# Kernel optimization log

Hardware: AMD Instinct MI355X
Metric: run time of the kernel (lower is better)

The kernel has to match this reference:

```python
import jax, jax.numpy as jnp
import numpy as np

ASPECT = 1.0
SCALE = 0.3
MIN_PATCH_H = 60.0
EPS = 1e-6


def _make_patch_boxes(boxes, H, W):
    # Patcher.create: per detected box, compute [ymin_patch, xmin_patch, patch_h, patch_w]
    ymin, xmin, ymax, xmax = jnp.split(boxes, 4, axis=-1)
    h = ymax - ymin
    w = xmax - xmin
    pw = h * SCALE
    ph = ASPECT * pw
    oy = ymin + h / 2.0
    ox = xmin + w / 2.0
    yp = jnp.maximum(oy - ph / 2.0, 0.0)
    xp = jnp.maximum(ox - pw / 2.0, 0.0)
    yp = jnp.where(yp + ph > H, H - ph, yp)
    xp = jnp.where(xp + pw > W, W - pw, xp)
    return jnp.concatenate([yp, xp, ph, pw], axis=-1)  # [B, N, 4]


def _bilinear(src, rel_y, rel_x, out_h, out_w):
    # tf.image.resize bilinear (half-pixel centers): sample src [P,P,3] at the
    # grid of an (out_h, out_w) resize, evaluated at all H/W image offsets.
    P = src.shape[0]
    sy = jnp.clip((rel_y + 0.5) * P / out_h - 0.5, 0.0, P - 1.0)  # [H]
    sx = jnp.clip((rel_x + 0.5) * P / out_w - 0.5, 0.0, P - 1.0)  # [W]
    y0 = jnp.floor(sy).astype(jnp.int32); y1 = jnp.minimum(y0 + 1, P - 1)
    x0 = jnp.floor(sx).astype(jnp.int32); x1 = jnp.minimum(x0 + 1, P - 1)
    wy = (sy - y0.astype(sy.dtype))[:, None, None]
    wx = (sx - x0.astype(sx.dtype))[None, :, None]
    top = (1.0 - wx) * src[y0[:, None], x0[None, :]] + wx * src[y0[:, None], x1[None, :]]
    bot = (1.0 - wx) * src[y1[:, None], x0[None, :]] + wx * src[y1[:, None], x1[None, :]]
    return (1.0 - wy) * top + wy * bot  # [H, W, 3]


def _forward(images, boxes, patch):
    B, H, W, _ = images.shape
    pboxes = _make_patch_boxes(boxes, float(H), float(W))  # [B, N, 4]
    valid = pboxes[..., 2] > MIN_PATCH_H                    # gather_nd filter
    p_mean = patch.mean((0, 1))
    p_std = patch.std((0, 1)) + EPS
    ys = jnp.arange(H, dtype=jnp.int32)
    xs = jnp.arange(W, dtype=jnp.int32)

    def per_image(image, pbs, vls):
        # serial while_loop over patches: later patches overwrite earlier ones,
        # and histogram match uses the current (already-patched) background.
        def step(img, bv):
            pb, v = bv
            pbi = pb.astype(jnp.int32)  # tf.cast truncation
            y0, x0, ph, pw = pbi[0], pbi[1], pbi[2], pbi[3]
            in_y = (ys >= y0) & (ys < y0 + ph)
            in_x = (xs >= x0) & (xs < x0 + pw)
            mask = in_y[:, None] & in_x[None, :]            # [H, W]
            mf = mask[..., None].astype(img.dtype)
            cnt = jnp.maximum(mask.sum().astype(img.dtype), 1.0)
            bg_mean = (img * mf).sum((0, 1)) / cnt
            bg_std = jnp.sqrt((((img - bg_mean) ** 2) * mf).sum((0, 1)) / cnt) + EPS
            # histogram match (per-channel moment matching) of patch to background
            matched = (patch - p_mean) / p_std * bg_std + bg_mean
            phf = jnp.maximum(ph.astype(img.dtype), 1.0)
            pwf = jnp.maximum(pw.astype(img.dtype), 1.0)
            sampled = _bilinear(matched,
                                (ys - y0).astype(img.dtype),
                                (xs - x0).astype(img.dtype), phf, pwf)
            img = jnp.where(mask[..., None] & v, sampled, img)
            return img, None

        img, _ = jax.lax.scan(step, image, (pbs, vls))
        return img

    return jax.vmap(per_image)(images, pboxes, valid)


def setup_inputs() -> dict:
    key = jax.random.key(0)
    k1, k2, k3 = jax.random.split(key, 3)
    B, N, H, W, P = 16, 16, 512, 512, 512
    images = jax.random.normal(k1, (B, H, W, 3), dtype=jnp.float32)
    u = jax.random.uniform(k2, (B, N, 4), dtype=jnp.float32)
    ymin = u[..., 0] * (H - 320)
    xmin = u[..., 1] * (W - 320)
    h = 150.0 + u[..., 2] * 150.0
    w = 150.0 + u[..., 3] * 150.0
    boxes = jnp.stack([ymin, xmin, ymin + h, xmin + w], axis=-1)
    patch = jax.random.normal(k3, (P, P, 3), dtype=jnp.float32) * 0.5
    return {"images": images, "boxes": boxes, "patch": patch}


def reference(images, boxes, patch):
    return _forward(images, boxes, patch)
```

## Files before the change

kernel.cpp:

```cpp
#include <hip/hip_runtime.h>
#include <math.h>

#define IMG_H 512
#define IMG_W 512
#define PSIZE 512
#define NIMG 16
#define NBOX 16
#define Z0 8
#define SLOTS 24
#define NTASK (256 * 17 * Z0)
#define NCOPY 2048
#define CHUNK4 1536
#define FBLOCKS 4096

#define WS_PMEAN 0
#define WS_PSTD  3
#define WS_PART  6
#define WS_PAIR  1544
#define WS_COEF  (1544 + 256 * SLOTS * 8)

typedef float f4u __attribute__((ext_vector_type(4), aligned(4)));
typedef float f2u __attribute__((ext_vector_type(2), aligned(4)));

struct BoxGeo { int y0, x0, ph, pw, valid; };

__device__ __forceinline__ BoxGeo make_geo(const float* bx) {
    float ymin = bx[0], xmin = bx[1], ymax = bx[2], xmax = bx[3];
    float h = ymax - ymin, w = xmax - xmin;
    float pwf = h * 0.3f;
    float phf = 1.0f * pwf;
    float oy = ymin + h * 0.5f;
    float ox = xmin + w * 0.5f;
    float yp = fmaxf(oy - phf * 0.5f, 0.0f);
    float xp = fmaxf(ox - pwf * 0.5f, 0.0f);
    if (yp + phf > (float)IMG_H) yp = (float)IMG_H - phf;
    if (xp + pwf > (float)IMG_W) xp = (float)IMG_W - pwf;
    BoxGeo g;
    g.y0 = (int)yp; g.x0 = (int)xp;
    g.ph = (int)phf; g.pw = (int)pwf;
    g.valid = (phf > 60.0f) ? 1 : 0;
    return g;
}

__device__ __forceinline__ void bsample_fast(const float* __restrict__ patch,
                                             int relY, int relX,
                                             float phf, float pwf, float s[3]) {
    float sy = ((float)relY + 0.5f) * (float)PSIZE / phf - 0.5f;
    sy = fminf(fmaxf(sy, 0.0f), (float)(PSIZE - 1));
    float sx = ((float)relX + 0.5f) * (float)PSIZE / pwf - 0.5f;
    sx = fminf(fmaxf(sx, 0.0f), (float)(PSIZE - 1));
    int y0 = (int)floorf(sy);
    int y1 = min(y0 + 1, PSIZE - 1);
    int x0 = (int)floorf(sx);
    float wy = sy - (float)y0;
    float wx = sx - (float)x0;
    const int baseX = min(x0, PSIZE - 2);
    const bool hi = (x0 == PSIZE - 1);
    const float* r0 = patch + (y0 * PSIZE + baseX) * 3;
    const float* r1 = patch + (y1 * PSIZE + baseX) * 3;
    f4u a0 = *(const f4u*)r0; f2u b0 = *(const f2u*)(r0 + 4);
    f4u a1 = *(const f4u*)r1; f2u b1 = *(const f2u*)(r1 + 4);
    float p00, p01, p10, p11, top, bot;
    p00 = hi ? a0.w : a0.x;  p01 = a0.w;
    p10 = hi ? a1.w : a1.x;  p11 = a1.w;
    top = (1.f - wx) * p00 + wx * p01; bot = (1.f - wx) * p10 + wx * p11;
    s[0] = (1.f - wy) * top + wy * bot;
    p00 = hi ? b0.x : a0.y;  p01 = b0.x;
    p10 = hi ? b1.x : a1.y;  p11 = b1.x;
    top = (1.f - wx) * p00 + wx * p01; bot = (1.f - wx) * p10 + wx * p11;
    s[1] = (1.f - wy) * top + wy * bot;
    p00 = hi ? b0.y : a0.z;  p01 = b0.y;
    p10 = hi ? b1.y : a1.z;  p11 = b1.y;
    top = (1.f - wx) * p00 + wx * p01; bot = (1.f - wx) * p10 + wx * p11;
    s[2] = (1.f - wy) * top + wy * bot;
}

template<int N, int NWAVES>
__device__ __forceinline__ void block_reduceN(float v[N]) {
    __shared__ float lds[NWAVES][N];
    const int lane = threadIdx.x & 63;
    const int wave = threadIdx.x >> 6;
    __syncthreads();
#pragma unroll
    for (int k = 0; k < N; ++k) {
#pragma unroll
        for (int off = 32; off > 0; off >>= 1)
            v[k] += __shfl_down(v[k], off, 64);
    }
    if (lane == 0) {
#pragma unroll
        for (int k = 0; k < N; ++k) lds[wave][k] = v[k];
    }
    __syncthreads();
    if (wave == 0) {
#pragma unroll
        for (int k = 0; k < N; ++k) {
            float x = (lane < NWAVES) ? lds[lane][k] : 0.0f;
#pragma unroll
            for (int off = 32; off > 0; off >>= 1)
                x += __shfl_down(x, off, 64);
            if (lane == 0) lds[0][k] = x;
        }
    }
    __syncthreads();
#pragma unroll
    for (int k = 0; k < N; ++k) v[k] = lds[0][k];
}

__global__ void patch_stats_partial(const float* __restrict__ patch,
                                    float* __restrict__ ws) {
    const int g = blockIdx.x * 256 + threadIdx.x;
    const float4* p4 = (const float4*)patch;
    float4 a = p4[3 * g], b = p4[3 * g + 1], c = p4[3 * g + 2];
    float v[6];
    v[0] = a.x + a.w + b.z + c.y;
    v[1] = a.y + b.x + b.w + c.z;
    v[2] = a.z + b.y + c.x + c.w;
    v[3] = a.x*a.x + a.w*a.w + b.z*b.z + c.y*c.y;
    v[4] = a.y*a.y + b.x*b.x + b.w*b.w + c.z*c.z;
    v[5] = a.z*a.z + b.y*b.y + c.x*c.x + c.w*c.w;
    block_reduceN<6, 4>(v);
    if (threadIdx.x == 0) {
        float* o = ws + WS_PART + blockIdx.x * 6;
#pragma unroll
        for (int k = 0; k < 6; ++k) o[k] = v[k];
    }
}

__launch_bounds__(256)
__global__ void fused(const float* __restrict__ images,
                      const float* __restrict__ boxes,
                      const float* __restrict__ patch,
                      float* __restrict__ ws,
                      float* __restrict__ out) {
    const int tid = threadIdx.x;
    __shared__ BoxGeo geo[NBOX];
    const int total = NTASK + NCOPY + 1;

    for (int it = blockIdx.x; it < total; it += FBLOCKS) {
        if (it >= NTASK) {
            if (it < NTASK + NCOPY) {
                const int c = it - NTASK;
                const float4* s4 = (const float4*)images;
                float4* d4 = (float4*)out;
                const int base = c * CHUNK4 + tid;
#pragma unroll
                for (int u = 0; u < 6; ++u)
                    d4[base + u * 256] = s4[base + u * 256];
            } else {
                float v[6];
                const float* p = ws + WS_PART + tid * 6;
#pragma unroll
                for (int k = 0; k < 6; ++k) v[k] = p[k];
                block_reduceN<6, 4>(v);
                if (tid == 0) {
                    const float n = (float)(PSIZE * PSIZE);
#pragma unroll
                    for (int c = 0; c < 3; ++c) {
                        float m = v[c] / n;
                        float var = v[3 + c] / n - m * m;
                        ws[WS_PMEAN + c] = m;
                        ws[WS_PSTD + c] = sqrtf(fmaxf(var, 0.f)) + 1e-6f;
                    }
                }
            }
            continue;
        }
        const int z = it / (17 * 256);
        const int rem = it % (17 * 256);
        const int j_idx = rem >> 8;
        const int bi = rem & 255;
        const int b = bi >> 4, i = bi & 15;
        if (j_idx > i) continue;
        if (j_idx >= 1 && z > 0) continue;

        const BoxGeo gi = make_geo(boxes + (b * NBOX + i) * 4);
        if (!gi.valid) continue;

        const int slot = (j_idx == 0) ? z : (Z0 + j_idx - 1);
        float* o = ws + WS_PAIR + ((size_t)bi * SLOTS + slot) * 8;

        int ry0 = gi.y0, rx0 = gi.x0;
        int ry1 = gi.y0 + gi.ph, rx1 = gi.x0 + gi.pw;
        int jy0 = 0, jx0 = 0, jph = -1;
        float jphf = 1.f, jpwf = 1.f;
        if (j_idx >= 1) {
            const BoxGeo gj = make_geo(boxes + (b * NBOX + j_idx - 1) * 4);
            if (!gj.valid) {
                if (tid == 0) { for (int k = 0; k < 7; ++k) o[k] = 0.f; }
                continue;
            }
            ry0 = max(ry0, gj.y0); rx0 = max(rx0, gj.x0);
            ry1 = min(ry1, gj.y0 + gj.ph); rx1 = min(rx1, gj.x0 + gj.pw);
            jy0 = gj.y0; jx0 = gj.x0; jph = gj.ph;
            jphf = (float)gj.ph; jpwf = (float)gj.pw;
        }
        const int rw = rx1 - rx0, rh = ry1 - ry0;
        if (rw <= 0 || rh <= 0) {
            if (tid == 0) { for (int k = 0; k < 7; ++k) o[k] = 0.f; }
            continue;
        }

        __syncthreads();
        if (tid < NBOX)
            geo[tid] = make_geo(boxes + (b * NBOX + tid) * 4);
        __syncthreads();

        const int n = rw * rh;
        const float* img = images + (size_t)b * IMG_H * IMG_W * 3;
        const int nz = (j_idx == 0) ? Z0 : 1;

        float v[7] = {0.f, 0.f, 0.f, 0.f, 0.f, 0.f, 0.f};
        for (int t = z * 256 + tid; t < n; t += 256 * nz) {
            const int y = ry0 + t / rw;
            const int x = rx0 + t % rw;
            bool inc = true;
            for (int k = j_idx; k < i; ++k) {
                const BoxGeo gk = geo[k];
                if (gk.valid && y >= gk.y0 && y < gk.y0 + gk.ph &&
                    x >= gk.x0 && x < gk.x0 + gk.pw) { inc = false; break; }
            }
            if (inc) {
                float s[3];
                if (jph > 0) {
                    bsample_fast(patch, y - jy0, x - jx0, jphf, jpwf, s);
                } else {
                    const float* p = img + ((size_t)y * IMG_W + x) * 3;
                    s[0] = p[0]; s[1] = p[1]; s[2] = p[2];
                }
                v[0] += 1.f;
                v[1] += s[0]; v[2] += s[1]; v[3] += s[2];
                v[4] += s[0]*s[0]; v[5] += s[1]*s[1]; v[6] += s[2]*s[2];
            }
        }
        block_reduceN<7, 4>(v);
        if (tid == 0) {
#pragma unroll
            for (int k = 0; k < 7; ++k) o[k] = v[k];
        }
    }
}

__global__ void solve_coeffs(const float* __restrict__ boxes,
                             float* __restrict__ ws) {
    const int b = blockIdx.x;
    const int lane = threadIdx.x;

    BoxGeo g = make_geo(boxes + (b * NBOX + (lane < NBOX ? lane : NBOX - 1)) * 4);
    float pm[3], ps[3];
#pragma unroll
    for (int c = 0; c < 3; ++c) { pm[c] = ws[WS_PMEAN + c]; ps[c] = ws[WS_PSTD + c]; }

    float sc[3] = {0.f, 0.f, 0.f}, of[3] = {0.f, 0.f, 0.f};

    for (int i = 0; i < NBOX; ++i) {
        const int valid_i = __shfl(g.valid, i, 64);
        if (!valid_i) continue;

        float cnt = 0.f, s1[3] = {0.f,0.f,0.f}, s2[3] = {0.f,0.f,0.f};
        if (lane <= i) {
            const int slot0 = (lane == 0) ? 0 : (Z0 + lane - 1);
            const int nz = (lane == 0) ? Z0 : 1;
            const float* p = ws + WS_PAIR +
                ((size_t)(b * NBOX + i) * SLOTS + slot0) * 8;
            for (int zz = 0; zz < nz; ++zz) {
                cnt   += p[zz*8 + 0];
                s1[0] += p[zz*8 + 1]; s1[1] += p[zz*8 + 2]; s1[2] += p[zz*8 + 3];
                s2[0] += p[zz*8 + 4]; s2[1] += p[zz*8 + 5]; s2[2] += p[zz*8 + 6];
            }
        }
        float ts[3], tq[3];
#pragma unroll
        for (int c = 0; c < 3; ++c) {
            if (lane == 0) { ts[c] = s1[c]; tq[c] = s2[c]; }
            else {
                ts[c] = sc[c] * s1[c] + of[c] * cnt;
                tq[c] = sc[c]*sc[c]*s2[c] + 2.f*sc[c]*of[c]*s1[c] + of[c]*of[c]*cnt;
            }
        }
#pragma unroll
        for (int c = 0; c < 3; ++c) {
#pragma unroll
            for (int off = 16; off > 0; off >>= 1) {
                ts[c] += __shfl_down(ts[c], off, 32);
                tq[c] += __shfl_down(tq[c], off, 32);
            }
        }
        const int phi = __shfl(g.ph, i, 64);
        const int pwi = __shfl(g.pw, i, 64);
        const float cntf = fmaxf((float)(phi * pwi), 1.0f);
        float nsc[3] = {0.f,0.f,0.f}, nof[3] = {0.f,0.f,0.f};
        if (lane == 0) {
#pragma unroll
            for (int c = 0; c < 3; ++c) {
                float mean = ts[c] / cntf;
                float var = tq[c] / cntf - mean * mean;
                float sd = sqrtf(fmaxf(var, 0.f)) + 1e-6f;
                nsc[c] = sd / ps[c];
                nof[c] = mean - pm[c] * nsc[c];
            }
        }
#pragma unroll
        for (int c = 0; c < 3; ++c) {
            float bs = __shfl(nsc[c], 0, 64);
            float bo = __shfl(nof[c], 0, 64);
            if (lane == i + 1) { sc[c] = bs; of[c] = bo; }
            if (lane == 0) {
                ws[WS_COEF + (size_t)(b * NBOX + i) * 8 + c] = bs;
                ws[WS_COEF + (size_t)(b * NBOX + i) * 8 + 3 + c] = bo;
            }
        }
    }
}

__launch_bounds__(256)
__global__ void decal(const float* __restrict__ boxes,
                      const float* __restrict__ patch,
                      const float* __restrict__ ws,
                      float* __restrict__ out) {
    const int bi = blockIdx.x;
    const int b = bi >> 4, i = bi & 15;
    const int z = blockIdx.y;
    __shared__ BoxGeo geo[NBOX];
    __shared__ float coef[6];
    if (threadIdx.x < NBOX)
        geo[threadIdx.x] = make_geo(boxes + (b * NBOX + threadIdx.x) * 4);
    if (threadIdx.x >= 32 && threadIdx.x < 38)
        coef[threadIdx.x - 32] = ws[WS_COEF + (size_t)bi * 8 + (threadIdx.x - 32)];
    __syncthreads();
    const BoxGeo gi = geo[i];
    if (!gi.valid) return;
    const int y0 = gi.y0, x0 = gi.x0, ph = gi.ph, pw = gi.pw;
    const int n = ph * pw;
    const float phf = (float)ph, pwf = (float)pw;
    float* img = out + (size_t)b * IMG_H * IMG_W * 3;

    for (int t = z * 256 + threadIdx.x; t < n; t += 256 * 8) {
        const int y = y0 + t / pw;
        const int x = x0 + t % pw;
        bool cov = false;
        for (int k = i + 1; k < NBOX; ++k) {
            const BoxGeo g = geo[k];
            if (g.valid && y >= g.y0 && y < g.y0 + g.ph &&
                x >= g.x0 && x < g.x0 + g.pw) { cov = true; break; }
        }
        if (!cov) {
            float s[3];
            bsample_fast(patch, y - y0, x - x0, phf, pwf, s);
            float* o = img + ((size_t)y * IMG_W + x) * 3;
            o[0] = s[0] * coef[0] + coef[3];
            o[1] = s[1] * coef[1] + coef[4];
            o[2] = s[2] * coef[2] + coef[5];
        }
    }
}

extern "C" void kernel_launch(void* const* d_in, const int* in_sizes, int n_in,
                              void* d_out, int out_size, void* d_ws, size_t ws_size,
                              hipStream_t stream) {
    const float* images = (const float*)d_in[0];
    const float* boxes  = (const float*)d_in[1];
    const float* patch  = (const float*)d_in[2];
    float* out = (float*)d_out;
    float* ws  = (float*)d_ws;

    patch_stats_partial<<<256, 256, 0, stream>>>(patch, ws);
    fused<<<FBLOCKS, 256, 0, stream>>>(images, boxes, patch, ws, out);
    solve_coeffs<<<NIMG, 64, 0, stream>>>(boxes, ws);
    decal<<<dim3(NIMG * NBOX, 8), 256, 0, stream>>>(boxes, patch, ws, out);
}
```

Baseline: 116.9 us.

## Merge four kernels into two and compact the fused task list

Folds the patch-statistics partial reduction into the first fused kernel as extra work items. It also replaces the sparse (z, j, bi) task grid, which had many early-exit items, with a dense enumeration: 8-way split tasks for the background stats plus 120 triangular pair tasks per image. The coefficient solve is merged into the decal kernel, so every decal block redundantly recomputes the final patch stats and the serial per-image coefficient chain up to its own box. This cuts two launches and removes wasted no-op iterations, at the cost of duplicated solve work in each of the 8 z-blocks per box.

```diff
diff --git a/kernel.cpp b/kernel.cpp
--- a/kernel.cpp
+++ b/kernel.cpp
@@ -8,16 +8,15 @@
 #define NBOX 16
 #define Z0 8
 #define SLOTS 24
-#define NTASK (256 * 17 * Z0)
-#define NCOPY 2048
-#define CHUNK4 1536
+#define IT_J0   256
+#define IT_PAIR 2304
+#define IT_COPY 4224
+#define NITEMS  6272
 #define FBLOCKS 4096
-
-#define WS_PMEAN 0
-#define WS_PSTD  3
-#define WS_PART  6
-#define WS_PAIR  1544
-#define WS_COEF  (1544 + 256 * SLOTS * 8)
+#define CHUNK4  1536
+
+#define WS_PART 0
+#define WS_PAIR 1536
 
 typedef float f4u __attribute__((ext_vector_type(4), aligned(4)));
 typedef float f2u __attribute__((ext_vector_type(2), aligned(4)));
@@ -107,85 +106,70 @@
     for (int k = 0; k < N; ++k) v[k] = lds[0][k];
 }
 
-__global__ void patch_stats_partial(const float* __restrict__ patch,
-                                    float* __restrict__ ws) {
-    const int g = blockIdx.x * 256 + threadIdx.x;
-    const float4* p4 = (const float4*)patch;
-    float4 a = p4[3 * g], b = p4[3 * g + 1], c = p4[3 * g + 2];
-    float v[6];
-    v[0] = a.x + a.w + b.z + c.y;
-    v[1] = a.y + b.x + b.w + c.z;
-    v[2] = a.z + b.y + c.x + c.w;
-    v[3] = a.x*a.x + a.w*a.w + b.z*b.z + c.y*c.y;
-    v[4] = a.y*a.y + b.x*b.x + b.w*b.w + c.z*c.z;
-    v[5] = a.z*a.z + b.y*b.y + c.x*c.x + c.w*c.w;
-    block_reduceN<6, 4>(v);
-    if (threadIdx.x == 0) {
-        float* o = ws + WS_PART + blockIdx.x * 6;
-#pragma unroll
-        for (int k = 0; k < 6; ++k) o[k] = v[k];
-    }
-}
-
 __launch_bounds__(256)
-__global__ void fused(const float* __restrict__ images,
-                      const float* __restrict__ boxes,
-                      const float* __restrict__ patch,
-                      float* __restrict__ ws,
-                      float* __restrict__ out) {
+__global__ void fused1(const float* __restrict__ images,
+                       const float* __restrict__ boxes,
+                       const float* __restrict__ patch,
+                       float* __restrict__ ws,
+                       float* __restrict__ out) {
     const int tid = threadIdx.x;
     __shared__ BoxGeo geo[NBOX];
-    const int total = NTASK + NCOPY + 1;
-
-    for (int it = blockIdx.x; it < total; it += FBLOCKS) {
-        if (it >= NTASK) {
-            if (it < NTASK + NCOPY) {
-                const int c = it - NTASK;
-                const float4* s4 = (const float4*)images;
-                float4* d4 = (float4*)out;
-                const int base = c * CHUNK4 + tid;
-#pragma unroll
-                for (int u = 0; u < 6; ++u)
-                    d4[base + u * 256] = s4[base + u * 256];
-            } else {
-                float v[6];
-                const float* p = ws + WS_PART + tid * 6;
-#pragma unroll
-                for (int k = 0; k < 6; ++k) v[k] = p[k];
-                block_reduceN<6, 4>(v);
-                if (tid == 0) {
-                    const float n = (float)(PSIZE * PSIZE);
-#pragma unroll
-                    for (int c = 0; c < 3; ++c) {
-                        float m = v[c] / n;
-                        float var = v[3 + c] / n - m * m;
-                        ws[WS_PMEAN + c] = m;
-                        ws[WS_PSTD + c] = sqrtf(fmaxf(var, 0.f)) + 1e-6f;
-                    }
-                }
+
+    for (int it = blockIdx.x; it < NITEMS; it += FBLOCKS) {
+        if (it < IT_J0) {
+            const int g = it * 256 + tid;
+            const float4* p4 = (const float4*)patch;
+            float4 a = p4[3 * g], b = p4[3 * g + 1], c = p4[3 * g + 2];
+            float v[6];
+            v[0] = a.x + a.w + b.z + c.y;
+            v[1] = a.y + b.x + b.w + c.z;
+            v[2] = a.z + b.y + c.x + c.w;
+            v[3] = a.x*a.x + a.w*a.w + b.z*b.z + c.y*c.y;
+            v[4] = a.y*a.y + b.x*b.x + b.w*b.w + c.z*c.z;
+            v[5] = a.z*a.z + b.y*b.y + c.x*c.x + c.w*c.w;
+            block_reduceN<6, 4>(v);
+            if (tid == 0) {
+                float* o = ws + WS_PART + it * 6;
+#pragma unroll
+                for (int k = 0; k < 6; ++k) o[k] = v[k];
             }
             continue;
         }
-        const int z = it / (17 * 256);
-        const int rem = it % (17 * 256);
-        const int j_idx = rem >> 8;
-        const int bi = rem & 255;
-        const int b = bi >> 4, i = bi & 15;
-        if (j_idx > i) continue;
-        if (j_idx >= 1 && z > 0) continue;
-
+        if (it >= IT_COPY) {
+            const int c = it - IT_COPY;
+            const float4* s4 = (const float4*)images;
+            float4* d4 = (float4*)out;
+            const int base = c * CHUNK4 + tid;
+#pragma unroll
+            for (int u = 0; u < 6; ++u)
+                d4[base + u * 256] = s4[base + u * 256];
+            continue;
+        }
+        int b, i, j, z;
+        if (it < IT_PAIR) {
+            const int idx = it - IT_J0;
+            const int bi = idx >> 3; z = idx & 7;
+            b = bi >> 4; i = bi & 15; j = -1;
+        } else {
+            const int idx = it - IT_PAIR;
+            b = idx / 120;
+            int p = idx % 120;
+            int pi = 1, t = p;
+            while (t >= pi) { t -= pi; ++pi; }
+            i = pi; j = t; z = 0;
+        }
         const BoxGeo gi = make_geo(boxes + (b * NBOX + i) * 4);
         if (!gi.valid) continue;
 
-        const int slot = (j_idx == 0) ? z : (Z0 + j_idx - 1);
-        float* o = ws + WS_PAIR + ((size_t)bi * SLOTS + slot) * 8;
+        const int slot = (j < 0) ? z : (Z0 + j);
+        float* o = ws + WS_PAIR + ((size_t)(b * NBOX + i) * SLOTS + slot) * 8;
 
         int ry0 = gi.y0, rx0 = gi.x0;
         int ry1 = gi.y0 + gi.ph, rx1 = gi.x0 + gi.pw;
         int jy0 = 0, jx0 = 0, jph = -1;
         float jphf = 1.f, jpwf = 1.f;
-        if (j_idx >= 1) {
-            const BoxGeo gj = make_geo(boxes + (b * NBOX + j_idx - 1) * 4);
+        if (j >= 0) {
+            const BoxGeo gj = make_geo(boxes + (b * NBOX + j) * 4);
             if (!gj.valid) {
                 if (tid == 0) { for (int k = 0; k < 7; ++k) o[k] = 0.f; }
                 continue;
@@ -208,14 +192,14 @@
 
         const int n = rw * rh;
         const float* img = images + (size_t)b * IMG_H * IMG_W * 3;
-        const int nz = (j_idx == 0) ? Z0 : 1;
+        const int stride = (j < 0) ? 256 * Z0 : 256;
 
         float v[7] = {0.f, 0.f, 0.f, 0.f, 0.f, 0.f, 0.f};
-        for (int t = z * 256 + tid; t < n; t += 256 * nz) {
+        for (int t = ((j < 0) ? z * 256 : 0) + tid; t < n; t += stride) {
             const int y = ry0 + t / rw;
             const int x = rx0 + t % rw;
             bool inc = true;
-            for (int k = j_idx; k < i; ++k) {
+            for (int k = j + 1; k < i; ++k) {
                 const BoxGeo gk = geo[k];
                 if (gk.valid && y >= gk.y0 && y < gk.y0 + gk.ph &&
                     x >= gk.x0 && x < gk.x0 + gk.pw) { inc = false; break; }
@@ -241,101 +225,113 @@
     }
 }
 
-__global__ void solve_coeffs(const float* __restrict__ boxes,
-                             float* __restrict__ ws) {
-    const int b = blockIdx.x;
-    const int lane = threadIdx.x;
-
-    BoxGeo g = make_geo(boxes + (b * NBOX + (lane < NBOX ? lane : NBOX - 1)) * 4);
-    float pm[3], ps[3];
-#pragma unroll
-    for (int c = 0; c < 3; ++c) { pm[c] = ws[WS_PMEAN + c]; ps[c] = ws[WS_PSTD + c]; }
-
-    float sc[3] = {0.f, 0.f, 0.f}, of[3] = {0.f, 0.f, 0.f};
-
-    for (int i = 0; i < NBOX; ++i) {
-        const int valid_i = __shfl(g.valid, i, 64);
-        if (!valid_i) continue;
-
-        float cnt = 0.f, s1[3] = {0.f,0.f,0.f}, s2[3] = {0.f,0.f,0.f};
-        if (lane <= i) {
-            const int slot0 = (lane == 0) ? 0 : (Z0 + lane - 1);
-            const int nz = (lane == 0) ? Z0 : 1;
-            const float* p = ws + WS_PAIR +
-                ((size_t)(b * NBOX + i) * SLOTS + slot0) * 8;
-            for (int zz = 0; zz < nz; ++zz) {
-                cnt   += p[zz*8 + 0];
-                s1[0] += p[zz*8 + 1]; s1[1] += p[zz*8 + 2]; s1[2] += p[zz*8 + 3];
-                s2[0] += p[zz*8 + 4]; s2[1] += p[zz*8 + 5]; s2[2] += p[zz*8 + 6];
-            }
-        }
-        float ts[3], tq[3];
+__launch_bounds__(256)
+__global__ void solve_decal(const float* __restrict__ boxes,
+                            const float* __restrict__ patch,
+                            const float* __restrict__ ws,
+                            float* __restrict__ out) {
+    const int bi = blockIdx.x;
+    const int z = blockIdx.y;
+    const int b = bi >> 4, i = bi & 15;
+    const int tid = threadIdx.x;
+    __shared__ BoxGeo geo[NBOX];
+    __shared__ float scoef[6];
+
+    if (tid < NBOX)
+        geo[tid] = make_geo(boxes + (b * NBOX + tid) * 4);
+    __syncthreads();
+    if (!geo[i].valid) return;
+
+    if (tid < 64) {
+        const int lane = tid;
+        float v[6] = {0.f, 0.f, 0.f, 0.f, 0.f, 0.f};
+        for (int q = lane; q < 256; q += 64) {
+            const float* p = ws + WS_PART + q * 6;
+#pragma unroll
+            for (int k = 0; k < 6; ++k) v[k] += p[k];
+        }
+#pragma unroll
+        for (int k = 0; k < 6; ++k)
+#pragma unroll
+            for (int off = 32; off > 0; off >>= 1)
+                v[k] += __shfl_xor(v[k], off, 64);
+        const float n = (float)(PSIZE * PSIZE);
+        float pm[3], ps[3];
 #pragma unroll
         for (int c = 0; c < 3; ++c) {
-            if (lane == 0) { ts[c] = s1[c]; tq[c] = s2[c]; }
-            else {
-                ts[c] = sc[c] * s1[c] + of[c] * cnt;
-                tq[c] = sc[c]*sc[c]*s2[c] + 2.f*sc[c]*of[c]*s1[c] + of[c]*of[c]*cnt;
-            }
-        }
-#pragma unroll
-        for (int c = 0; c < 3; ++c) {
-#pragma unroll
-            for (int off = 16; off > 0; off >>= 1) {
-                ts[c] += __shfl_down(ts[c], off, 32);
-                tq[c] += __shfl_down(tq[c], off, 32);
-            }
-        }
-        const int phi = __shfl(g.ph, i, 64);
-        const int pwi = __shfl(g.pw, i, 64);
-        const float cntf = fmaxf((float)(phi * pwi), 1.0f);
-        float nsc[3] = {0.f,0.f,0.f}, nof[3] = {0.f,0.f,0.f};
-        if (lane == 0) {
+            pm[c] = v[c] / n;
+            ps[c] = sqrtf(fmaxf(v[3 + c] / n - pm[c] * pm[c], 0.f)) + 1e-6f;
+        }
+
+        BoxGeo g = geo[lane & 15];
+        float sc[3] = {0.f, 0.f, 0.f}, of[3] = {0.f, 0.f, 0.f};
+
+        for (int ii = 0; ii <= i; ++ii) {
+            const int valid_i = __shfl(g.valid, ii, 64);
+            if (!valid_i) continue;
+
+            float cnt = 0.f, s1[3] = {0.f,0.f,0.f}, s2[3] = {0.f,0.f,0.f};
+            if (lane <= ii) {
+                const int slot0 = (lane == 0) ? 0 : (Z0 + lane - 1);
+                const int nzz = (lane == 0) ? Z0 : 1;
+                const float* p = ws + WS_PAIR +
+                    ((size_t)(b * NBOX + ii) * SLOTS + slot0) * 8;
+                for (int zz = 0; zz < nzz; ++zz) {
+                    cnt   += p[zz*8 + 0];
+                    s1[0] += p[zz*8 + 1]; s1[1] += p[zz*8 + 2]; s1[2] += p[zz*8 + 3];
+                    s2[0] += p[zz*8 + 4]; s2[1] += p[zz*8 + 5]; s2[2] += p[zz*8 + 6];
+                }
+            }
+            float ts[3], tq[3];
 #pragma unroll
             for (int c = 0; c < 3; ++c) {
-                float mean = ts[c] / cntf;
-                float var = tq[c] / cntf - mean * mean;
-                float sd = sqrtf(fmaxf(var, 0.f)) + 1e-6f;
-                nsc[c] = sd / ps[c];
-                nof[c] = mean - pm[c] * nsc[c];
-            }
-        }
-#pragma unroll
-        for (int c = 0; c < 3; ++c) {
-            float bs = __shfl(nsc[c], 0, 64);
-            float bo = __shfl(nof[c], 0, 64);
-            if (lane == i + 1) { sc[c] = bs; of[c] = bo; }
+                if (lane == 0) { ts[c] = s1[c]; tq[c] = s2[c]; }
+                else {
+                    ts[c] = sc[c] * s1[c] + of[c] * cnt;
+                    tq[c] = sc[c]*sc[c]*s2[c] + 2.f*sc[c]*of[c]*s1[c]
+                          + of[c]*of[c]*cnt;
+                }
+            }
+#pragma unroll
+            for (int c = 0; c < 3; ++c) {
+#pragma unroll
+                for (int off = 16; off > 0; off >>= 1) {
+                    ts[c] += __shfl_down(ts[c], off, 32);
+                    tq[c] += __shfl_down(tq[c], off, 32);
+                }
+            }
+            const int phi = __shfl(g.ph, ii, 64);
+            const int pwi = __shfl(g.pw, ii, 64);
+            const float cntf = fmaxf((float)(phi * pwi), 1.0f);
+            float nsc[3] = {0.f,0.f,0.f}, nof[3] = {0.f,0.f,0.f};
             if (lane == 0) {
-                ws[WS_COEF + (size_t)(b * NBOX + i) * 8 + c] = bs;
-                ws[WS_COEF + (size_t)(b * NBOX + i) * 8 + 3 + c] = bo;
-            }
-        }
-    }
-}
-
-__launch_bounds__(256)
-__global__ void decal(const float* __restrict__ boxes,
-                      const float* __restrict__ patch,
-                      const float* __restrict__ ws,
-                      float* __restrict__ out) {
-    const int bi = blockIdx.x;
-    const int b = bi >> 4, i = bi & 15;
-    const int z = blockIdx.y;
-    __shared__ BoxGeo geo[NBOX];
-    __shared__ float coef[6];
-    if (threadIdx.x < NBOX)
-        geo[threadIdx.x] = make_geo(boxes + (b * NBOX + threadIdx.x) * 4);
-    if (threadIdx.x >= 32 && threadIdx.x < 38)
-        coef[threadIdx.x - 32] = ws[WS_COEF + (size_t)bi * 8 + (threadIdx.x - 32)];
-    __syncthreads();
+#pragma unroll
+                for (int c = 0; c < 3; ++c) {
+                    float mean = ts[c] / cntf;
+                    float var = tq[c] / cntf - mean * mean;
+                    float sd = sqrtf(fmaxf(var, 0.f)) + 1e-6f;
+                    nsc[c] = sd / ps[c];
+                    nof[c] = mean - pm[c] * nsc[c];
+                }
+            }
+#pragma unroll
+            for (int c = 0; c < 3; ++c) {
+                float bs = __shfl(nsc[c], 0, 64);
+                float bo = __shfl(nof[c], 0, 64);
+                if (lane == ii + 1) { sc[c] = bs; of[c] = bo; }
+                if (ii == i && lane == 0) { scoef[c] = bs; scoef[3 + c] = bo; }
+            }
+        }
+    }
+    __syncthreads();
+
     const BoxGeo gi = geo[i];
-    if (!gi.valid) return;
     const int y0 = gi.y0, x0 = gi.x0, ph = gi.ph, pw = gi.pw;
     const int n = ph * pw;
     const float phf = (float)ph, pwf = (float)pw;
     float* img = out + (size_t)b * IMG_H * IMG_W * 3;
 
-    for (int t = z * 256 + threadIdx.x; t < n; t += 256 * 8) {
+    for (int t = z * 256 + tid; t < n; t += 256 * 8) {
         const int y = y0 + t / pw;
         const int x = x0 + t % pw;
         bool cov = false;
@@ -348,9 +344,9 @@
             float s[3];
             bsample_fast(patch, y - y0, x - x0, phf, pwf, s);
             float* o = img + ((size_t)y * IMG_W + x) * 3;
-            o[0] = s[0] * coef[0] + coef[3];
-            o[1] = s[1] * coef[1] + coef[4];
-            o[2] = s[2] * coef[2] + coef[5];
+            o[0] = s[0] * scoef[0] + scoef[3];
+            o[1] = s[1] * scoef[1] + scoef[4];
+            o[2] = s[2] * scoef[2] + scoef[5];
         }
     }
 }
@@ -364,8 +360,6 @@
     float* out = (float*)d_out;
     float* ws  = (float*)d_ws;
 
-    patch_stats_partial<<<256, 256, 0, stream>>>(patch, ws);
-    fused<<<FBLOCKS, 256, 0, stream>>>(images, boxes, patch, ws, out);
-    solve_coeffs<<<NIMG, 64, 0, stream>>>(boxes, ws);
-    decal<<<dim3(NIMG * NBOX, 8), 256, 0, stream>>>(boxes, patch, ws, out);
-}
+    fused1<<<FBLOCKS, 256, 0, stream>>>(images, boxes, patch, ws, out);
+    solve_decal<<<dim3(NIMG * NBOX, 8), 256, 0, stream>>>(boxes, patch, ws, out);
+}
```

Result: faster. 101.9 us (-12.8%).
